# Kernel optimization log

Hardware: AMD Instinct MI355X
Metric: run time of the kernel (lower is better)

Reference implementation:

```python
import jax, jax.numpy as jnp
import numpy as np

EPS = 1e-5  # torch LayerNorm default

def ln(x, g, b):
    mu = jnp.mean(x, axis=-1, keepdims=True)
    var = jnp.mean((x - mu) ** 2, axis=-1, keepdims=True)
    return (x - mu) * jax.lax.rsqrt(var + EPS) * g + b

B, S, E, A = 131072, 199, 3, 32
D_IN = S + 1  # state_dim + 1 (time feature)

def setup_inputs() -> dict:
    key = jax.random.key(0)
    ks = iter(jax.random.split(key, 32))
    def w(shape, fan_in):
        lim = 1.0 / np.sqrt(fan_in)
        return jax.random.uniform(next(ks), shape, jnp.float32, -lim, lim)
    inp = {
        "state": jax.random.normal(next(ks), (B, S), jnp.float32),
        "time_delta": jax.random.uniform(next(ks), (B,), jnp.float32),
        # trunk: Linear(200,256)+LN, Linear(256,256)+LN, Linear(256,128)+LN
        "W1": w((D_IN, 256), D_IN), "b1": w((256,), D_IN),
        "g1": jnp.ones((256,), jnp.float32), "be1": jnp.zeros((256,), jnp.float32),
        "W2": w((256, 256), 256), "b2": w((256,), 256),
        "g2": jnp.ones((256,), jnp.float32), "be2": jnp.zeros((256,), jnp.float32),
        "W3": w((256, 128), 256), "b3": w((128,), 256),
        "g3": jnp.ones((128,), jnp.float32), "be3": jnp.zeros((128,), jnp.float32),
        # value stream
        "Wv1": w((128, 64), 128), "bv1": w((64,), 128),
        "gv": jnp.ones((64,), jnp.float32), "bev": jnp.zeros((64,), jnp.float32),
        "Wv2": w((64, 1), 64), "bv2": w((1,), 64),
        # E stacked advantage streams (all heads share action dim A)
        "Wa1": w((E, 128, 64), 128), "ba1": w((E, 64), 128),
        "ga": jnp.ones((E, 64), jnp.float32), "bea": jnp.zeros((E, 64), jnp.float32),
        "Wa2": w((E, 64, A), 64), "ba2": w((E, A), 64),
        "event_type": jax.random.randint(next(ks), (B,), 0, E),
    }
    return inp

def reference(state, time_delta,
              W1, b1, g1, be1, W2, b2, g2, be2, W3, b3, g3, be3,
              Wv1, bv1, gv, bev, Wv2, bv2,
              Wa1, ba1, ga, bea, Wa2, ba2, event_type):
    td = time_delta[:, None]                       # [B,1]
    x = jnp.concatenate([state, td], axis=1)       # [B,200]
    h = jax.nn.relu(ln(x @ W1 + b1, g1, be1))      # [B,256]
    h = jax.nn.relu(ln(h @ W2 + b2, g2, be2))      # [B,256]
    f = jax.nn.relu(ln(h @ W3 + b3, g3, be3))      # [B,128]
    v = jax.nn.relu(ln(f @ Wv1 + bv1, gv, bev)) @ Wv2 + bv2  # [B,1]
    # compute all E advantage heads, then per-sample select by event_type
    h1 = jnp.einsum('bd,edh->ebh', f, Wa1) + ba1[:, None, :]           # [E,B,64]
    h1 = jax.nn.relu(ln(h1, ga[:, None, :], bea[:, None, :]))
    adv_all = jnp.einsum('ebh,eha->eba', h1, Wa2) + ba2[:, None, :]    # [E,B,A]
    adv = jnp.take_along_axis(adv_all, event_type[None, :, None], axis=0)[0]  # [B,A]
    return v + (adv - adv.mean(axis=1, keepdims=True))
```

## Files before the change

### kernel.cpp

```cpp
#include <hip/hip_runtime.h>
#include <hip/hip_bf16.h>
#include <stdint.h>

#define DEV __device__ __forceinline__

typedef __attribute__((ext_vector_type(8))) short short8;
typedef __attribute__((ext_vector_type(4))) float floatx4;

constexpr int TM  = 64;
constexpr int NB  = 131072;
constexpr int AST = 264;

constexpr int OFF_W1 = 0;
constexpr int OFF_W2 = 57344;
constexpr int OFF_W3 = 122880;
constexpr int OFF_WH = 155648;
constexpr int OFF_WA2= 188416;
constexpr int NWQ    = 194560;

constexpr int C_B1=0, C_G1=256, C_BE1=512, C_B2=768, C_G2=1024, C_BE2=1280,
  C_B3=1536, C_G3=1664, C_BE3=1792, C_BV1=1920, C_GV=1984, C_BEV=2048,
  C_WV2=2112, C_BV2=2176, C_BA1=2180, C_GA=2372, C_BEA=2564, C_BA2=2756;
constexpr int NCONST=2852;

struct Ptrs {
  const float *state,*td,*W1,*b1,*g1,*be1,*W2,*b2,*g2,*be2,*W3,*b3,*g3,*be3,
    *Wv1,*bv1,*gv,*bev,*Wv2,*bv2,*Wa1,*ba1,*ga,*bea,*Wa2,*ba2;
  const int *et;
};

DEV unsigned short f2bf(float x){
  uint32_t u = __float_as_uint(x);
  u += 0x7fffu + ((u>>16)&1u);
  return (unsigned short)(u>>16);
}
DEV uint32_t f2bf_pk(float a, float b){
  float2 f2; f2.x=a; f2.y=b;
  __hip_bfloat162 h = __float22bfloat162_rn(f2);
  union { __hip_bfloat162 h; uint32_t u; } cv; cv.h = h;
  return cv.u;
}

__global__ void prep_kernel(Ptrs p, unsigned short* __restrict__ wq, float* __restrict__ cq){
  int idx = blockIdx.x*256 + threadIdx.x;
  if (idx < NWQ) {
    float v = 0.f;
    if (idx < OFF_W2) {
      int e = idx, w = e/14336, r = e%14336;
      int kc = r>>11, ct=(r>>9)&3, l=(r>>3)&63, j=r&7;
      int n = w*64 + ct*16 + (l&15);
      int k = kc*32 + (l>>4)*8 + j;
      if (k < 200) v = p.W1[k*256 + n];
      else if (k == 200) v = p.b1[n];
    } else if (idx < OFF_W3) {
      int e = idx-OFF_W2, w=e>>14, r=e&16383;
      int kc=r>>11, ct=(r>>9)&3, l=(r>>3)&63, j=r&7;
      int n = w*64 + ct*16 + (l&15);
      int k = kc*32 + (l>>4)*8 + j;
      v = p.W2[k*256 + n];
    } else if (idx < OFF_WH) {
      int e = idx-OFF_W3, w=e>>13, r=e&8191;
      int kc=r>>10, ct=(r>>9)&1, l=(r>>3)&63, j=r&7;
      int n = w*32 + ct*16 + (l&15);
      int k = kc*32 + (l>>4)*8 + j;
      v = p.W3[k*128 + n];
    } else if (idx < OFF_WA2) {
      int e = idx-OFF_WH, h=e>>13, r=e&8191;
      int kc=r>>11, ct=(r>>9)&3, l=(r>>3)&63, j=r&7;
      int n = ct*16 + (l&15);
      int k = kc*32 + (l>>4)*8 + j;
      v = (h<3) ? p.Wa1[h*8192 + k*64 + n] : p.Wv1[k*64 + n];
    } else {
      int e = idx-OFF_WA2, h=e>>11, r=e&2047;
      int kc=r>>10, ct=(r>>9)&1, l=(r>>3)&63, j=r&7;
      int n = ct*16 + (l&15);
      int k = kc*32 + (l>>4)*8 + j;
      v = p.Wa2[h*2048 + k*32 + n];
    }
    wq[idx] = f2bf(v);
  } else if (idx < NWQ + NCONST) {
    int ci = idx - NWQ;
    float v;
    if      (ci < 256)  v = p.b1[ci];
    else if (ci < 512)  v = p.g1[ci-256];
    else if (ci < 768)  v = p.be1[ci-512];
    else if (ci < 1024) v = p.b2[ci-768];
    else if (ci < 1280) v = p.g2[ci-1024];
    else if (ci < 1536) v = p.be2[ci-1280];
    else if (ci < 1664) v = p.b3[ci-1536];
    else if (ci < 1792) v = p.g3[ci-1664];
    else if (ci < 1920) v = p.be3[ci-1792];
    else if (ci < 1984) v = p.bv1[ci-1920];
    else if (ci < 2048) v = p.gv[ci-1984];
    else if (ci < 2112) v = p.bev[ci-2048];
    else if (ci < 2176) v = p.Wv2[ci-2112];
    else if (ci < 2180) v = (ci==2176) ? p.bv2[0] : 0.f;
    else if (ci < 2372) v = p.ba1[ci-2180];
    else if (ci < 2564) v = p.ga[ci-2372];
    else if (ci < 2756) v = p.bea[ci-2564];
    else                v = p.ba2[ci-2756];
    cq[ci] = v;
  }
}

template<int RT,int CT>
DEV void zeroAccT(floatx4 (&acc)[RT][CT]){
  const floatx4 z = {0.f,0.f,0.f,0.f};
  #pragma unroll
  for (int rt=0;rt<RT;rt++)
    #pragma unroll
    for (int ct=0;ct<CT;ct++) acc[rt][ct]=z;
}

template<int KC,int RT,int CT>
DEV void runGemmTW(floatx4 (&acc)[RT][CT], const unsigned short* __restrict__ wp, int kcStride,
                   const unsigned short* aB, int aOff, int lane){
  #pragma unroll
  for (int kc=0;kc<KC;kc++){
    short8 a[CT];
    #pragma unroll
    for (int c=0;c<CT;c++)
      a[c] = *(const short8*)(aB + c*16*AST + aOff + kc*32);
    #pragma unroll
    for (int rt=0;rt<RT;rt++){
      short8 bw = *(const short8*)(wp + kc*kcStride + rt*512 + lane*8);
      #pragma unroll
      for (int c=0;c<CT;c++)
        acc[rt][c] = __builtin_amdgcn_mfma_f32_16x16x32_bf16(bw, a[c], acc[rt][c], 0,0,0);
    }
  }
}

template<int RT,bool BIAS>
DEV void statsT(floatx4 (&acc)[RT][4], const float* __restrict__ cq, int bo,
                float* sbuf, float* ssbuf, int q, int ln){
  if constexpr (BIAS){
    #pragma unroll
    for (int rt=0;rt<RT;rt++){
      floatx4 b4 = *(const floatx4*)(cq + bo + rt*16 + q*4);
      #pragma unroll
      for (int ct=0;ct<4;ct++) acc[rt][ct] += b4;
    }
  }
  #pragma unroll
  for (int ct=0;ct<4;ct++){
    float s=0.f, ss=0.f;
    #pragma unroll
    for (int rt=0;rt<RT;rt++)
      #pragma unroll
      for (int r=0;r<4;r++){ float v=acc[rt][ct][r]; s+=v; ss+=v*v; }
    s += __shfl_xor(s,16); ss += __shfl_xor(ss,16);
    s += __shfl_xor(s,32); ss += __shfl_xor(ss,32);
    if (q==0){
      atomicAdd(&sbuf[ct*16+ln], s);
      atomicAdd(&ssbuf[ct*16+ln], ss);
    }
  }
}

template<int RT>
DEV void lnWriteT(const floatx4 (&acc)[RT][4], const float* __restrict__ cq, int go, int beo,
                  const float* sbuf, const float* ssbuf, float invN,
                  unsigned short* act_, int colBase, int q, int ln){
  float mu[4], rs[4];
  #pragma unroll
  for (int ct=0;ct<4;ct++){
    float sv = sbuf[ct*16+ln], ssv = ssbuf[ct*16+ln];
    mu[ct] = sv*invN;
    rs[ct] = rsqrtf(ssv*invN - mu[ct]*mu[ct] + 1e-5f);
  }
  #pragma unroll
  for (int rt=0;rt<RT;rt++){
    floatx4 g4  = *(const floatx4*)(cq + go  + rt*16 + q*4);
    floatx4 be4 = *(const floatx4*)(cq + beo + rt*16 + q*4);
    #pragma unroll
    for (int ct=0;ct<4;ct++){
      float y[4];
      #pragma unroll
      for (int r=0;r<4;r++)
        y[r] = fmaxf((acc[rt][ct][r]-mu[ct])*rs[ct]*g4[r]+be4[r], 0.f);
      uint2 pk; pk.x = f2bf_pk(y[0],y[1]); pk.y = f2bf_pk(y[2],y[3]);
      *(uint2*)(act_ + (ct*16+ln)*AST + colBase + rt*16 + q*4) = pk;
    }
  }
}

__global__ __launch_bounds__(512,6) void dqn_main(
    const float* __restrict__ state, const float* __restrict__ td,
    const int* __restrict__ et, const unsigned short* __restrict__ wq,
    const float* __restrict__ cq, float* __restrict__ out)
{
  __shared__ __align__(16) unsigned short act[TM*AST];
  __shared__ float sstat[2][2][64];
  __shared__ float vbuf[64];
  __shared__ int   etl[64];

  const int tid=threadIdx.x, w=tid>>6, lane=tid&63, q=lane>>4, ln=lane&15;
  const int rowBlk = blockIdx.x*TM;

  {
    if (tid < 256) ((float*)sstat)[tid] = 0.f;
    const float* sbase = state + (size_t)rowBlk*199;
    #pragma unroll
    for (int it=0; it<4; ++it){
      int t = tid + it*512;
      if (t < 1792){
        int r = t/28, c = t - r*28;
        unsigned short* dst = act + r*AST + c*8;
        if (c < 25){
          const float* src = sbase + r*199 + c*8;
          float v0=src[0], v1=src[1], v2=src[2], v3=src[3];
          float v4=src[4], v5=src[5], v6=src[6];
          int o7 = (c==24)? 198 : c*8+7;
          float s7 = sbase[r*199 + o7];
          float v7 = (c==24)? td[rowBlk+r] : s7;
          uint4 pk;
          pk.x=f2bf_pk(v0,v1); pk.y=f2bf_pk(v2,v3);
          pk.z=f2bf_pk(v4,v5); pk.w=f2bf_pk(v6,v7);
          *(uint4*)dst = pk;
        } else {
          uint4 pk{0u,0u,0u,0u};
          if (c==25) pk.x = 0x3F80u;
          *(uint4*)dst = pk;
        }
      }
    }
    if (tid < 64) etl[tid] = et[rowBlk+tid];
  }
  __syncthreads();

  const unsigned short* aBase = act + ln*AST + q*8;
  floatx4 acc[2][4];

  {
    const unsigned short* wp = wq + OFF_W1 + (w>>1)*14336 + (w&1)*1024;
    zeroAccT<2,4>(acc);
    runGemmTW<7,2,4>(acc, wp, 2048, aBase, 0, lane);
  }
  statsT<2,false>(acc, cq, 0, sstat[0][0], sstat[0][1], q, ln);
  __syncthreads();
  lnWriteT<2>(acc, cq, C_G1+w*32, C_BE1+w*32, sstat[0][0], sstat[0][1], 1.f/256.f, act, w*32, q, ln);
  __syncthreads();

  {
    const unsigned short* wp = wq + OFF_W2 + (w>>1)*16384 + (w&1)*1024;
    zeroAccT<2,4>(acc);
    runGemmTW<8,2,4>(acc, wp, 2048, aBase, 0, lane);
  }
  statsT<2,true>(acc, cq, C_B2+w*32, sstat[1][0], sstat[1][1], q, ln);
  __syncthreads();
  if (tid < 128) ((float*)sstat[0])[tid] = 0.f;
  lnWriteT<2>(acc, cq, C_G2+w*32, C_BE2+w*32, sstat[1][0], sstat[1][1], 1.f/256.f, act, w*32, q, ln);
  __syncthreads();

  floatx4 acc3[1][4];
  {
    const unsigned short* wp = wq + OFF_W3 + (w>>1)*8192 + (w&1)*512;
    zeroAccT<1,4>(acc3);
    runGemmTW<8,1,4>(acc3, wp, 1024, aBase, 0, lane);
  }
  statsT<1,true>(acc3, cq, C_B3+w*16, sstat[0][0], sstat[0][1], q, ln);
  __syncthreads();
  lnWriteT<1>(acc3, cq, C_G3+w*16, C_BE3+w*16, sstat[0][0], sstat[0][1], 1.f/128.f, act, w*16, q, ln);
  __syncthreads();

  const int h = w>>1, bh = w&1;
  const unsigned short* aBaseH = act + (bh*32 + ln)*AST + q*8;
  floatx4 acch[4][2];
  {
    const unsigned short* wp = wq + OFF_WH + h*8192;
    zeroAccT<4,2>(acch);
    runGemmTW<4,4,2>(acch, wp, 2048, aBaseH, 0, lane);
  }
  {
    const int bo = (h<3)? C_BA1+h*64 : C_BV1;
    const int go = (h<3)? C_GA +h*64 : C_GV;
    const int beo= (h<3)? C_BEA+h*64 : C_BEV;
    #pragma unroll
    for (int rt=0;rt<4;rt++){
      floatx4 b4 = *(const floatx4*)(cq + bo + rt*16 + q*4);
      #pragma unroll
      for (int ct=0;ct<2;ct++) acch[rt][ct] += b4;
    }
    float mu[2], rs[2];
    #pragma unroll
    for (int ct=0;ct<2;ct++){
      float s=0.f, ss=0.f;
      #pragma unroll
      for (int rt=0;rt<4;rt++)
        #pragma unroll
        for (int r=0;r<4;r++){ float v=acch[rt][ct][r]; s+=v; ss+=v*v; }
      s += __shfl_xor(s,16); ss += __shfl_xor(ss,16);
      s += __shfl_xor(s,32); ss += __shfl_xor(ss,32);
      mu[ct]=s*(1.f/64.f);
      rs[ct]=rsqrtf(ss*(1.f/64.f)-mu[ct]*mu[ct]+1e-5f);
    }
    #pragma unroll
    for (int rt=0;rt<4;rt++){
      floatx4 g4  = *(const floatx4*)(cq + go  + rt*16 + q*4);
      floatx4 be4 = *(const floatx4*)(cq + beo + rt*16 + q*4);
      #pragma unroll
      for (int ct=0;ct<2;ct++)
        #pragma unroll
        for (int r=0;r<4;r++)
          acch[rt][ct][r] = fmaxf((acch[rt][ct][r]-mu[ct])*rs[ct]*g4[r]+be4[r], 0.f);
    }
    if (h==3){
      float bv2v = cq[C_BV2];
      floatx4 wv4[4];
      #pragma unroll
      for (int rt=0;rt<4;rt++) wv4[rt] = *(const floatx4*)(cq + C_WV2 + rt*16 + q*4);
      #pragma unroll
      for (int ct=0;ct<2;ct++){
        float dot=0.f;
        #pragma unroll
        for (int rt=0;rt<4;rt++)
          #pragma unroll
          for (int r=0;r<4;r++) dot += acch[rt][ct][r]*wv4[rt][r];
        dot += __shfl_xor(dot,16);
        dot += __shfl_xor(dot,32);
        if (q==0) vbuf[(bh*2+ct)*16+ln] = dot + bv2v;
      }
    }
  }
  __syncthreads();

  if (h<3){
    #pragma unroll
    for (int rt=0;rt<4;rt++)
      #pragma unroll
      for (int ct=0;ct<2;ct++){
        uint2 pk;
        pk.x = f2bf_pk(acch[rt][ct][0], acch[rt][ct][1]);
        pk.y = f2bf_pk(acch[rt][ct][2], acch[rt][ct][3]);
        *(uint2*)(act + ((bh*2+ct)*16+ln)*AST + 64*h + rt*16 + q*4) = pk;
      }
    floatx4 acc2[2][2];
    {
      const unsigned short* wp = wq + OFF_WA2 + h*2048;
      zeroAccT<2,2>(acc2);
      runGemmTW<2,2,2>(acc2, wp, 1024, aBaseH, 64*h, lane);
    }
    #pragma unroll
    for (int rt=0;rt<2;rt++){
      floatx4 b4 = *(const floatx4*)(cq + C_BA2 + h*32 + rt*16 + q*4);
      #pragma unroll
      for (int ct=0;ct<2;ct++) acc2[rt][ct] += b4;
    }
    #pragma unroll
    for (int ct=0;ct<2;ct++){
      float sm=0.f;
      #pragma unroll
      for (int rt=0;rt<2;rt++)
        #pragma unroll
        for (int r=0;r<4;r++) sm += acc2[rt][ct][r];
      sm += __shfl_xor(sm,16);
      sm += __shfl_xor(sm,32);
      int b = (bh*2+ct)*16+ln;
      if (etl[b]==h){
        float vm = vbuf[b] - sm*(1.f/32.f);
        #pragma unroll
        for (int rt=0;rt<2;rt++){
          floatx4 o = acc2[rt][ct];
          o[0]+=vm; o[1]+=vm; o[2]+=vm; o[3]+=vm;
          *(floatx4*)(out + (size_t)(rowBlk+b)*32 + rt*16 + q*4) = o;
        }
      }
    }
  }
}

extern "C" void kernel_launch(void* const* d_in, const int* in_sizes, int n_in,
                              void* d_out, int out_size, void* d_ws, size_t ws_size,
                              hipStream_t stream)
{
  Ptrs p;
  p.state=(const float*)d_in[0];  p.td =(const float*)d_in[1];
  p.W1 =(const float*)d_in[2];  p.b1 =(const float*)d_in[3];  p.g1 =(const float*)d_in[4];  p.be1=(const float*)d_in[5];
  p.W2 =(const float*)d_in[6];  p.b2 =(const float*)d_in[7];  p.g2 =(const float*)d_in[8];  p.be2=(const float*)d_in[9];
  p.W3 =(const float*)d_in[10]; p.b3 =(const float*)d_in[11]; p.g3 =(const float*)d_in[12]; p.be3=(const float*)d_in[13];
  p.Wv1=(const float*)d_in[14]; p.bv1=(const float*)d_in[15]; p.gv =(const float*)d_in[16]; p.bev=(const float*)d_in[17];
  p.Wv2=(const float*)d_in[18]; p.bv2=(const float*)d_in[19];
  p.Wa1=(const float*)d_in[20]; p.ba1=(const float*)d_in[21]; p.ga =(const float*)d_in[22]; p.bea=(const float*)d_in[23];
  p.Wa2=(const float*)d_in[24]; p.ba2=(const float*)d_in[25];
  p.et =(const int*)d_in[26];

  unsigned short* wq = (unsigned short*)d_ws;
  float* cq = (float*)((char*)d_ws + (size_t)NWQ*2);

  const int prepN = NWQ + NCONST;
  hipLaunchKernelGGL(prep_kernel, dim3((prepN+255)/256), dim3(256), 0, stream, p, wq, cq);
  hipLaunchKernelGGL(dqn_main, dim3(NB/TM), dim3(512), 0, stream,
                     p.state, p.td, p.et, (const unsigned short*)wq, (const float*)cq, (float*)d_out);
}
```

Before: 287.0 us.

## Rewrite MLP as register-resident per-wave 32-row pipeline using 32x32 MFMA

Replaces the block-cooperative LDS-staged design with one where each wave owns 32 batch rows and keeps activations entirely in registers. Layers use 32x32x16 bf16 MFMA, with LayerNorm stats reduced within the wave, and permlane32 swaps repack outputs into B fragments for the next layer. Biases are folded into the weight matrices as an extra K row. This removes LDS round-trips, atomics and block barriers between layers, at the cost of heavy register pressure at 2 blocks of 256 threads and every wave streaming the full weight set from global/L2.

```diff
diff --git a/kernel.cpp b/kernel.cpp
--- a/kernel.cpp
+++ b/kernel.cpp
@@ -5,23 +5,21 @@
 #define DEV __device__ __forceinline__
 
 typedef __attribute__((ext_vector_type(8))) short short8;
+typedef __attribute__((ext_vector_type(16))) float f32x16;
 typedef __attribute__((ext_vector_type(4))) float floatx4;
 
-constexpr int TM  = 64;
-constexpr int NB  = 131072;
-constexpr int AST = 264;
+constexpr int NB = 131072;
 
 constexpr int OFF_W1 = 0;
-constexpr int OFF_W2 = 57344;
+constexpr int OFF_W2 = 53248;
 constexpr int OFF_W3 = 122880;
-constexpr int OFF_WH = 155648;
-constexpr int OFF_WA2= 188416;
-constexpr int NWQ    = 194560;
-
-constexpr int C_B1=0, C_G1=256, C_BE1=512, C_B2=768, C_G2=1024, C_BE2=1280,
-  C_B3=1536, C_G3=1664, C_BE3=1792, C_BV1=1920, C_GV=1984, C_BEV=2048,
-  C_WV2=2112, C_BV2=2176, C_BA1=2180, C_GA=2372, C_BEA=2564, C_BA2=2756;
-constexpr int NCONST=2852;
+constexpr int OFF_WH = 157696;
+constexpr int OFF_WA2= 194560;
+constexpr int NWQ    = 202240;
+
+constexpr int C_G1=0, C_BE1=256, C_G2=512, C_BE2=768, C_G3=1024, C_BE3=1152,
+  C_GH=1280, C_BEH=1536, C_WV2=1792, C_BV2=1856;
+constexpr int NCONST=1860;
 
 struct Ptrs {
   const float *state,*td,*W1,*b1,*g1,*be1,*W2,*b2,*g2,*be2,*W3,*b3,*g3,*be3,
@@ -34,7 +32,7 @@
   u += 0x7fffu + ((u>>16)&1u);
   return (unsigned short)(u>>16);
 }
-DEV uint32_t f2bf_pk(float a, float b){
+DEV uint32_t pkbf(float a, float b){
   float2 f2; f2.x=a; f2.y=b;
   __hip_bfloat162 h = __float22bfloat162_rn(f2);
   union { __hip_bfloat162 h; uint32_t u; } cv; cv.h = h;
@@ -46,325 +44,318 @@
   if (idx < NWQ) {
     float v = 0.f;
     if (idx < OFF_W2) {
-      int e = idx, w = e/14336, r = e%14336;
-      int kc = r>>11, ct=(r>>9)&3, l=(r>>3)&63, j=r&7;
-      int n = w*64 + ct*16 + (l&15);
-      int k = kc*32 + (l>>4)*8 + j;
+      int e=idx, kc=e>>12, li=e&4095, nt=li>>9, l=(li>>3)&63, j=li&7;
+      int k = kc*16 + (l>>5)*8 + j, n = nt*32 + (l&31);
       if (k < 200) v = p.W1[k*256 + n];
       else if (k == 200) v = p.b1[n];
     } else if (idx < OFF_W3) {
-      int e = idx-OFF_W2, w=e>>14, r=e&16383;
-      int kc=r>>11, ct=(r>>9)&3, l=(r>>3)&63, j=r&7;
-      int n = w*64 + ct*16 + (l&15);
-      int k = kc*32 + (l>>4)*8 + j;
-      v = p.W2[k*256 + n];
+      int e=idx-OFF_W2, kc=e>>12, li=e&4095, nt=li>>9, l=(li>>3)&63, j=li&7;
+      int k = kc*16 + (l>>5)*8 + j, n = nt*32 + (l&31);
+      if (k < 256) v = p.W2[k*256 + n];
+      else if (k == 256) v = p.b2[n];
     } else if (idx < OFF_WH) {
-      int e = idx-OFF_W3, w=e>>13, r=e&8191;
-      int kc=r>>10, ct=(r>>9)&1, l=(r>>3)&63, j=r&7;
-      int n = w*32 + ct*16 + (l&15);
-      int k = kc*32 + (l>>4)*8 + j;
-      v = p.W3[k*128 + n];
+      int e=idx-OFF_W3, kc=e>>11, li=e&2047, nt=li>>9, l=(li>>3)&63, j=li&7;
+      int k = kc*16 + (l>>5)*8 + j, n = nt*32 + (l&31);
+      if (k < 256) v = p.W3[k*128 + n];
+      else if (k == 256) v = p.b3[n];
     } else if (idx < OFF_WA2) {
-      int e = idx-OFF_WH, h=e>>13, r=e&8191;
-      int kc=r>>11, ct=(r>>9)&3, l=(r>>3)&63, j=r&7;
-      int n = ct*16 + (l&15);
-      int k = kc*32 + (l>>4)*8 + j;
-      v = (h<3) ? p.Wa1[h*8192 + k*64 + n] : p.Wv1[k*64 + n];
+      int e=idx-OFF_WH, kc=e>>12, li=e&4095, nt=li>>9, l=(li>>3)&63, j=li&7;
+      int k = kc*16 + (l>>5)*8 + j;
+      int h = nt>>1, nl = (nt&1)*32 + (l&31);
+      if (k < 128) v = (h<3) ? p.Wa1[h*8192 + k*64 + nl] : p.Wv1[k*64 + nl];
+      else if (k == 128) v = (h<3) ? p.ba1[h*64 + nl] : p.bv1[nl];
     } else {
-      int e = idx-OFF_WA2, h=e>>11, r=e&2047;
-      int kc=r>>10, ct=(r>>9)&1, l=(r>>3)&63, j=r&7;
-      int n = ct*16 + (l&15);
-      int k = kc*32 + (l>>4)*8 + j;
-      v = p.Wa2[h*2048 + k*32 + n];
+      int e=idx-OFF_WA2, kc=e/1536, li=e%1536, h=li>>9, l=(li>>3)&63, j=li&7;
+      int k = kc*16 + (l>>5)*8 + j, nl = l&31;
+      if (k < 64) v = p.Wa2[h*2048 + k*32 + nl];
+      else if (k == 64) v = p.ba2[h*32 + nl];
     }
     wq[idx] = f2bf(v);
   } else if (idx < NWQ + NCONST) {
-    int ci = idx - NWQ;
-    float v;
-    if      (ci < 256)  v = p.b1[ci];
-    else if (ci < 512)  v = p.g1[ci-256];
-    else if (ci < 768)  v = p.be1[ci-512];
-    else if (ci < 1024) v = p.b2[ci-768];
-    else if (ci < 1280) v = p.g2[ci-1024];
-    else if (ci < 1536) v = p.be2[ci-1280];
-    else if (ci < 1664) v = p.b3[ci-1536];
-    else if (ci < 1792) v = p.g3[ci-1664];
-    else if (ci < 1920) v = p.be3[ci-1792];
-    else if (ci < 1984) v = p.bv1[ci-1920];
-    else if (ci < 2048) v = p.gv[ci-1984];
-    else if (ci < 2112) v = p.bev[ci-2048];
-    else if (ci < 2176) v = p.Wv2[ci-2112];
-    else if (ci < 2180) v = (ci==2176) ? p.bv2[0] : 0.f;
-    else if (ci < 2372) v = p.ba1[ci-2180];
-    else if (ci < 2564) v = p.ga[ci-2372];
-    else if (ci < 2756) v = p.bea[ci-2564];
-    else                v = p.ba2[ci-2756];
+    int ci = idx - NWQ; float v = 0.f;
+    if      (ci < 256)  v = p.g1[ci];
+    else if (ci < 512)  v = p.be1[ci-256];
+    else if (ci < 768)  v = p.g2[ci-512];
+    else if (ci < 1024) v = p.be2[ci-768];
+    else if (ci < 1152) v = p.g3[ci-1024];
+    else if (ci < 1280) v = p.be3[ci-1152];
+    else if (ci < 1536) { int i=ci-1280; v = (i<192)? p.ga[i]  : p.gv[i-192]; }
+    else if (ci < 1792) { int i=ci-1536; v = (i<192)? p.bea[i] : p.bev[i-192]; }
+    else if (ci < 1856) v = p.Wv2[ci-1792];
+    else if (ci ==1856) v = p.bv2[0];
     cq[ci] = v;
   }
 }
 
-template<int RT,int CT>
-DEV void zeroAccT(floatx4 (&acc)[RT][CT]){
-  const floatx4 z = {0.f,0.f,0.f,0.f};
-  #pragma unroll
-  for (int rt=0;rt<RT;rt++)
-    #pragma unroll
-    for (int ct=0;ct<CT;ct++) acc[rt][ct]=z;
-}
-
-template<int KC,int RT,int CT>
-DEV void runGemmTW(floatx4 (&acc)[RT][CT], const unsigned short* __restrict__ wp, int kcStride,
-                   const unsigned short* aB, int aOff, int lane){
-  #pragma unroll
-  for (int kc=0;kc<KC;kc++){
-    short8 a[CT];
-    #pragma unroll
-    for (int c=0;c<CT;c++)
-      a[c] = *(const short8*)(aB + c*16*AST + aOff + kc*32);
-    #pragma unroll
-    for (int rt=0;rt<RT;rt++){
-      short8 bw = *(const short8*)(wp + kc*kcStride + rt*512 + lane*8);
-      #pragma unroll
-      for (int c=0;c<CT;c++)
-        acc[rt][c] = __builtin_amdgcn_mfma_f32_16x16x32_bf16(bw, a[c], acc[rt][c], 0,0,0);
-    }
-  }
-}
-
-template<int RT,bool BIAS>
-DEV void statsT(floatx4 (&acc)[RT][4], const float* __restrict__ cq, int bo,
-                float* sbuf, float* ssbuf, int q, int ln){
-  if constexpr (BIAS){
-    #pragma unroll
-    for (int rt=0;rt<RT;rt++){
-      floatx4 b4 = *(const floatx4*)(cq + bo + rt*16 + q*4);
-      #pragma unroll
-      for (int ct=0;ct<4;ct++) acc[rt][ct] += b4;
-    }
-  }
-  #pragma unroll
-  for (int ct=0;ct<4;ct++){
-    float s=0.f, ss=0.f;
-    #pragma unroll
-    for (int rt=0;rt<RT;rt++)
-      #pragma unroll
-      for (int r=0;r<4;r++){ float v=acc[rt][ct][r]; s+=v; ss+=v*v; }
-    s += __shfl_xor(s,16); ss += __shfl_xor(ss,16);
-    s += __shfl_xor(s,32); ss += __shfl_xor(ss,32);
-    if (q==0){
-      atomicAdd(&sbuf[ct*16+ln], s);
-      atomicAdd(&ssbuf[ct*16+ln], ss);
-    }
-  }
-}
-
-template<int RT>
-DEV void lnWriteT(const floatx4 (&acc)[RT][4], const float* __restrict__ cq, int go, int beo,
-                  const float* sbuf, const float* ssbuf, float invN,
-                  unsigned short* act_, int colBase, int q, int ln){
-  float mu[4], rs[4];
-  #pragma unroll
-  for (int ct=0;ct<4;ct++){
-    float sv = sbuf[ct*16+ln], ssv = ssbuf[ct*16+ln];
-    mu[ct] = sv*invN;
-    rs[ct] = rsqrtf(ssv*invN - mu[ct]*mu[ct] + 1e-5f);
-  }
-  #pragma unroll
-  for (int rt=0;rt<RT;rt++){
-    floatx4 g4  = *(const floatx4*)(cq + go  + rt*16 + q*4);
-    floatx4 be4 = *(const floatx4*)(cq + beo + rt*16 + q*4);
-    #pragma unroll
-    for (int ct=0;ct<4;ct++){
-      float y[4];
-      #pragma unroll
-      for (int r=0;r<4;r++)
-        y[r] = fmaxf((acc[rt][ct][r]-mu[ct])*rs[ct]*g4[r]+be4[r], 0.f);
-      uint2 pk; pk.x = f2bf_pk(y[0],y[1]); pk.y = f2bf_pk(y[2],y[3]);
-      *(uint2*)(act_ + (ct*16+ln)*AST + colBase + rt*16 + q*4) = pk;
-    }
-  }
-}
-
-__global__ __launch_bounds__(512,6) void dqn_main(
+DEV floatx4 ld4(const float* p){ return *(const floatx4*)p; }
+
+DEV short8 mk_frag(uint32_t w0, uint32_t w1, uint32_t w2, uint32_t w3){
+  union { uint32_t u[4]; short8 s; } cv;
+  cv.u[0]=w0; cv.u[1]=w1; cv.u[2]=w2; cv.u[3]=w3; return cv.s;
+}
+DEV void pl32swap(uint32_t &x, uint32_t &y){
+  asm volatile("v_permlane32_swap_b32 %0, %1" : "+v"(x), "+v"(y));
+}
+DEV f32x16 mf(short8 a, short8 b, f32x16 c){
+  return __builtin_amdgcn_mfma_f32_32x32x16_bf16(a, b, c, 0, 0, 0);
+}
+
+DEV void tile_to_frags(const float (&y)[16], short8 &f0, short8 &f1){
+  uint32_t P0 = pkbf(y[0], y[1]), P1 = pkbf(y[2], y[3]);
+  uint32_t Q0 = pkbf(y[4], y[5]), Q1 = pkbf(y[6], y[7]);
+  pl32swap(P0, Q0); pl32swap(P1, Q1);
+  f0 = mk_frag(P0, P1, Q0, Q1);
+  uint32_t R0 = pkbf(y[8], y[9]),  R1 = pkbf(y[10], y[11]);
+  uint32_t S0 = pkbf(y[12], y[13]),S1 = pkbf(y[14], y[15]);
+  pl32swap(R0, S0); pl32swap(R1, S1);
+  f1 = mk_frag(R0, R1, S0, S1);
+}
+
+__global__ __launch_bounds__(256,2) void dqn_main(
     const float* __restrict__ state, const float* __restrict__ td,
     const int* __restrict__ et, const unsigned short* __restrict__ wq,
     const float* __restrict__ cq, float* __restrict__ out)
 {
-  __shared__ __align__(16) unsigned short act[TM*AST];
-  __shared__ float sstat[2][2][64];
-  __shared__ float vbuf[64];
-  __shared__ int   etl[64];
-
-  const int tid=threadIdx.x, w=tid>>6, lane=tid&63, q=lane>>4, ln=lane&15;
-  const int rowBlk = blockIdx.x*TM;
-
-  {
-    if (tid < 256) ((float*)sstat)[tid] = 0.f;
-    const float* sbase = state + (size_t)rowBlk*199;
-    #pragma unroll
-    for (int it=0; it<4; ++it){
-      int t = tid + it*512;
-      if (t < 1792){
-        int r = t/28, c = t - r*28;
-        unsigned short* dst = act + r*AST + c*8;
-        if (c < 25){
-          const float* src = sbase + r*199 + c*8;
-          float v0=src[0], v1=src[1], v2=src[2], v3=src[3];
-          float v4=src[4], v5=src[5], v6=src[6];
-          int o7 = (c==24)? 198 : c*8+7;
-          float s7 = sbase[r*199 + o7];
-          float v7 = (c==24)? td[rowBlk+r] : s7;
-          uint4 pk;
-          pk.x=f2bf_pk(v0,v1); pk.y=f2bf_pk(v2,v3);
-          pk.z=f2bf_pk(v4,v5); pk.w=f2bf_pk(v6,v7);
-          *(uint4*)dst = pk;
+  const int tid = threadIdx.x, wv = tid>>6, l = tid&63;
+  const int hi = l>>5, c = l&31;
+  const int b = blockIdx.x*128 + wv*32 + c;
+
+  const float* sph = state + (size_t)b*199 + hi*8;
+  const float  tdv = td[b];
+  const int    etv = et[b];
+
+  const f32x16 z16 = {0,0,0,0,0,0,0,0,0,0,0,0,0,0,0,0};
+  const short8 bias_bf = mk_frag(hi==0 ? 0x3F80u : 0u, 0u, 0u, 0u);
+
+  f32x16 acc[8];
+
+  {
+    #pragma unroll
+    for (int t=0;t<8;t++) acc[t] = z16;
+    const unsigned short* wl = wq + OFF_W1 + l*8;
+    #pragma unroll
+    for (int kc=0;kc<13;kc++){
+      short8 bf;
+      if (kc < 12){
+        float v0=sph[kc*16+0], v1=sph[kc*16+1], v2=sph[kc*16+2], v3=sph[kc*16+3];
+        float v4=sph[kc*16+4], v5=sph[kc*16+5], v6=sph[kc*16+6], v7=sph[kc*16+7];
+        bf = mk_frag(pkbf(v0,v1), pkbf(v2,v3), pkbf(v4,v5), pkbf(v6,v7));
+      } else {
+        if (hi == 0){
+          float v0=sph[192], v1=sph[193], v2=sph[194], v3=sph[195];
+          float v4=sph[196], v5=sph[197], v6=sph[198], v7=tdv;
+          bf = mk_frag(pkbf(v0,v1), pkbf(v2,v3), pkbf(v4,v5), pkbf(v6,v7));
         } else {
-          uint4 pk{0u,0u,0u,0u};
-          if (c==25) pk.x = 0x3F80u;
-          *(uint4*)dst = pk;
-        }
-      }
-    }
-    if (tid < 64) etl[tid] = et[rowBlk+tid];
-  }
-  __syncthreads();
-
-  const unsigned short* aBase = act + ln*AST + q*8;
-  floatx4 acc[2][4];
-
-  {
-    const unsigned short* wp = wq + OFF_W1 + (w>>1)*14336 + (w&1)*1024;
-    zeroAccT<2,4>(acc);
-    runGemmTW<7,2,4>(acc, wp, 2048, aBase, 0, lane);
-  }
-  statsT<2,false>(acc, cq, 0, sstat[0][0], sstat[0][1], q, ln);
-  __syncthreads();
-  lnWriteT<2>(acc, cq, C_G1+w*32, C_BE1+w*32, sstat[0][0], sstat[0][1], 1.f/256.f, act, w*32, q, ln);
-  __syncthreads();
-
-  {
-    const unsigned short* wp = wq + OFF_W2 + (w>>1)*16384 + (w&1)*1024;
-    zeroAccT<2,4>(acc);
-    runGemmTW<8,2,4>(acc, wp, 2048, aBase, 0, lane);
-  }
-  statsT<2,true>(acc, cq, C_B2+w*32, sstat[1][0], sstat[1][1], q, ln);
-  __syncthreads();
-  if (tid < 128) ((float*)sstat[0])[tid] = 0.f;
-  lnWriteT<2>(acc, cq, C_G2+w*32, C_BE2+w*32, sstat[1][0], sstat[1][1], 1.f/256.f, act, w*32, q, ln);
-  __syncthreads();
-
-  floatx4 acc3[1][4];
-  {
-    const unsigned short* wp = wq + OFF_W3 + (w>>1)*8192 + (w&1)*512;
-    zeroAccT<1,4>(acc3);
-    runGemmTW<8,1,4>(acc3, wp, 1024, aBase, 0, lane);
-  }
-  statsT<1,true>(acc3, cq, C_B3+w*16, sstat[0][0], sstat[0][1], q, ln);
-  __syncthreads();
-  lnWriteT<1>(acc3, cq, C_G3+w*16, C_BE3+w*16, sstat[0][0], sstat[0][1], 1.f/128.f, act, w*16, q, ln);
-  __syncthreads();
-
-  const int h = w>>1, bh = w&1;
-  const unsigned short* aBaseH = act + (bh*32 + ln)*AST + q*8;
-  floatx4 acch[4][2];
-  {
-    const unsigned short* wp = wq + OFF_WH + h*8192;
-    zeroAccT<4,2>(acch);
-    runGemmTW<4,4,2>(acch, wp, 2048, aBaseH, 0, lane);
-  }
-  {
-    const int bo = (h<3)? C_BA1+h*64 : C_BV1;
-    const int go = (h<3)? C_GA +h*64 : C_GV;
-    const int beo= (h<3)? C_BEA+h*64 : C_BEV;
-    #pragma unroll
-    for (int rt=0;rt<4;rt++){
-      floatx4 b4 = *(const floatx4*)(cq + bo + rt*16 + q*4);
-      #pragma unroll
-      for (int ct=0;ct<2;ct++) acch[rt][ct] += b4;
-    }
-    float mu[2], rs[2];
-    #pragma unroll
-    for (int ct=0;ct<2;ct++){
-      float s=0.f, ss=0.f;
-      #pragma unroll
-      for (int rt=0;rt<4;rt++)
-        #pragma unroll
-        for (int r=0;r<4;r++){ float v=acch[rt][ct][r]; s+=v; ss+=v*v; }
-      s += __shfl_xor(s,16); ss += __shfl_xor(ss,16);
-      s += __shfl_xor(s,32); ss += __shfl_xor(ss,32);
-      mu[ct]=s*(1.f/64.f);
-      rs[ct]=rsqrtf(ss*(1.f/64.f)-mu[ct]*mu[ct]+1e-5f);
-    }
-    #pragma unroll
-    for (int rt=0;rt<4;rt++){
-      floatx4 g4  = *(const floatx4*)(cq + go  + rt*16 + q*4);
-      floatx4 be4 = *(const floatx4*)(cq + beo + rt*16 + q*4);
-      #pragma unroll
-      for (int ct=0;ct<2;ct++)
-        #pragma unroll
-        for (int r=0;r<4;r++)
-          acch[rt][ct][r] = fmaxf((acch[rt][ct][r]-mu[ct])*rs[ct]*g4[r]+be4[r], 0.f);
-    }
-    if (h==3){
-      float bv2v = cq[C_BV2];
-      floatx4 wv4[4];
-      #pragma unroll
-      for (int rt=0;rt<4;rt++) wv4[rt] = *(const floatx4*)(cq + C_WV2 + rt*16 + q*4);
-      #pragma unroll
-      for (int ct=0;ct<2;ct++){
-        float dot=0.f;
-        #pragma unroll
-        for (int rt=0;rt<4;rt++)
-          #pragma unroll
-          for (int r=0;r<4;r++) dot += acch[rt][ct][r]*wv4[rt][r];
-        dot += __shfl_xor(dot,16);
-        dot += __shfl_xor(dot,32);
-        if (q==0) vbuf[(bh*2+ct)*16+ln] = dot + bv2v;
-      }
-    }
-  }
-  __syncthreads();
-
-  if (h<3){
-    #pragma unroll
-    for (int rt=0;rt<4;rt++)
-      #pragma unroll
-      for (int ct=0;ct<2;ct++){
-        uint2 pk;
-        pk.x = f2bf_pk(acch[rt][ct][0], acch[rt][ct][1]);
-        pk.y = f2bf_pk(acch[rt][ct][2], acch[rt][ct][3]);
-        *(uint2*)(act + ((bh*2+ct)*16+ln)*AST + 64*h + rt*16 + q*4) = pk;
-      }
-    floatx4 acc2[2][2];
-    {
-      const unsigned short* wp = wq + OFF_WA2 + h*2048;
-      zeroAccT<2,2>(acc2);
-      runGemmTW<2,2,2>(acc2, wp, 1024, aBaseH, 64*h, lane);
-    }
-    #pragma unroll
-    for (int rt=0;rt<2;rt++){
-      floatx4 b4 = *(const floatx4*)(cq + C_BA2 + h*32 + rt*16 + q*4);
-      #pragma unroll
-      for (int ct=0;ct<2;ct++) acc2[rt][ct] += b4;
-    }
-    #pragma unroll
-    for (int ct=0;ct<2;ct++){
-      float sm=0.f;
-      #pragma unroll
-      for (int rt=0;rt<2;rt++)
-        #pragma unroll
-        for (int r=0;r<4;r++) sm += acc2[rt][ct][r];
-      sm += __shfl_xor(sm,16);
-      sm += __shfl_xor(sm,32);
-      int b = (bh*2+ct)*16+ln;
-      if (etl[b]==h){
-        float vm = vbuf[b] - sm*(1.f/32.f);
-        #pragma unroll
-        for (int rt=0;rt<2;rt++){
-          floatx4 o = acc2[rt][ct];
-          o[0]+=vm; o[1]+=vm; o[2]+=vm; o[3]+=vm;
-          *(floatx4*)(out + (size_t)(rowBlk+b)*32 + rt*16 + q*4) = o;
-        }
+          bf = mk_frag(0x3F80u, 0u, 0u, 0u);
+        }
+      }
+      #pragma unroll
+      for (int nt=0;nt<8;nt++)
+        acc[nt] = mf(*(const short8*)(wl + (kc*8+nt)*512), bf, acc[nt]);
+    }
+  }
+
+  short8 Bf[16];
+  {
+    float s=0.f, ss=0.f;
+    #pragma unroll
+    for (int t=0;t<8;t++)
+      #pragma unroll
+      for (int r=0;r<16;r++){ float v=acc[t][r]; s+=v; ss+=v*v; }
+    s += __shfl_xor(s,32); ss += __shfl_xor(ss,32);
+    float mu = s*(1.f/256.f);
+    float rsv = rsqrtf(ss*(1.f/256.f) - mu*mu + 1e-5f);
+    float mrs = mu*rsv;
+    #pragma unroll
+    for (int t=0;t<8;t++){
+      float y[16];
+      #pragma unroll
+      for (int m=0;m<4;m++){
+        floatx4 g4 = ld4(cq + C_G1  + t*32 + m*8 + hi*4);
+        floatx4 e4 = ld4(cq + C_BE1 + t*32 + m*8 + hi*4);
+        #pragma unroll
+        for (int rr=0;rr<4;rr++){
+          float tv = fmaf(acc[t][m*4+rr], rsv, -mrs);
+          y[m*4+rr] = fmaxf(fmaf(tv, g4[rr], e4[rr]), 0.f);
+        }
+      }
+      tile_to_frags(y, Bf[t*2], Bf[t*2+1]);
+    }
+  }
+
+  {
+    #pragma unroll
+    for (int t=0;t<8;t++) acc[t] = z16;
+    const unsigned short* wl = wq + OFF_W2 + l*8;
+    #pragma unroll
+    for (int kc=0;kc<17;kc++){
+      short8 bf = (kc<16) ? Bf[kc] : bias_bf;
+      #pragma unroll
+      for (int nt=0;nt<8;nt++)
+        acc[nt] = mf(*(const short8*)(wl + (kc*8+nt)*512), bf, acc[nt]);
+    }
+  }
+
+  {
+    float s=0.f, ss=0.f;
+    #pragma unroll
+    for (int t=0;t<8;t++)
+      #pragma unroll
+      for (int r=0;r<16;r++){ float v=acc[t][r]; s+=v; ss+=v*v; }
+    s += __shfl_xor(s,32); ss += __shfl_xor(ss,32);
+    float mu = s*(1.f/256.f);
+    float rsv = rsqrtf(ss*(1.f/256.f) - mu*mu + 1e-5f);
+    float mrs = mu*rsv;
+    #pragma unroll
+    for (int t=0;t<8;t++){
+      float y[16];
+      #pragma unroll
+      for (int m=0;m<4;m++){
+        floatx4 g4 = ld4(cq + C_G2  + t*32 + m*8 + hi*4);
+        floatx4 e4 = ld4(cq + C_BE2 + t*32 + m*8 + hi*4);
+        #pragma unroll
+        for (int rr=0;rr<4;rr++){
+          float tv = fmaf(acc[t][m*4+rr], rsv, -mrs);
+          y[m*4+rr] = fmaxf(fmaf(tv, g4[rr], e4[rr]), 0.f);
+        }
+      }
+      tile_to_frags(y, Bf[t*2], Bf[t*2+1]);
+    }
+  }
+
+  {
+    #pragma unroll
+    for (int t=0;t<4;t++) acc[t] = z16;
+    const unsigned short* wl = wq + OFF_W3 + l*8;
+    #pragma unroll
+    for (int kc=0;kc<17;kc++){
+      short8 bf = (kc<16) ? Bf[kc] : bias_bf;
+      #pragma unroll
+      for (int nt=0;nt<4;nt++)
+        acc[nt] = mf(*(const short8*)(wl + (kc*4+nt)*512), bf, acc[nt]);
+    }
+  }
+
+  short8 Ff[8];
+  {
+    float s=0.f, ss=0.f;
+    #pragma unroll
+    for (int t=0;t<4;t++)
+      #pragma unroll
+      for (int r=0;r<16;r++){ float v=acc[t][r]; s+=v; ss+=v*v; }
+    s += __shfl_xor(s,32); ss += __shfl_xor(ss,32);
+    float mu = s*(1.f/128.f);
+    float rsv = rsqrtf(ss*(1.f/128.f) - mu*mu + 1e-5f);
+    float mrs = mu*rsv;
+    #pragma unroll
+    for (int t=0;t<4;t++){
+      float y[16];
+      #pragma unroll
+      for (int m=0;m<4;m++){
+        floatx4 g4 = ld4(cq + C_G3  + t*32 + m*8 + hi*4);
+        floatx4 e4 = ld4(cq + C_BE3 + t*32 + m*8 + hi*4);
+        #pragma unroll
+        for (int rr=0;rr<4;rr++){
+          float tv = fmaf(acc[t][m*4+rr], rsv, -mrs);
+          y[m*4+rr] = fmaxf(fmaf(tv, g4[rr], e4[rr]), 0.f);
+        }
+      }
+      tile_to_frags(y, Ff[t*2], Ff[t*2+1]);
+    }
+  }
+
+  {
+    #pragma unroll
+    for (int t=0;t<8;t++) acc[t] = z16;
+    const unsigned short* wl = wq + OFF_WH + l*8;
+    #pragma unroll
+    for (int kc=0;kc<9;kc++){
+      short8 bf = (kc<8) ? Ff[kc] : bias_bf;
+      #pragma unroll
+      for (int nt=0;nt<8;nt++)
+        acc[nt] = mf(*(const short8*)(wl + (kc*8+nt)*512), bf, acc[nt]);
+    }
+  }
+
+  float vval;
+  {
+    float s=0.f, ss=0.f;
+    #pragma unroll
+    for (int t=6;t<8;t++)
+      #pragma unroll
+      for (int r=0;r<16;r++){ float v=acc[t][r]; s+=v; ss+=v*v; }
+    s += __shfl_xor(s,32); ss += __shfl_xor(ss,32);
+    float mu = s*(1.f/64.f);
+    float rsv = rsqrtf(ss*(1.f/64.f) - mu*mu + 1e-5f);
+    float mrs = mu*rsv;
+    float dot = 0.f;
+    #pragma unroll
+    for (int t=6;t<8;t++)
+      #pragma unroll
+      for (int m=0;m<4;m++){
+        floatx4 g4 = ld4(cq + C_GH  + t*32 + m*8 + hi*4);
+        floatx4 e4 = ld4(cq + C_BEH + t*32 + m*8 + hi*4);
+        floatx4 w4 = ld4(cq + C_WV2 + (t-6)*32 + m*8 + hi*4);
+        #pragma unroll
+        for (int rr=0;rr<4;rr++){
+          float tv = fmaf(acc[t][m*4+rr], rsv, -mrs);
+          float y  = fmaxf(fmaf(tv, g4[rr], e4[rr]), 0.f);
+          dot = fmaf(y, w4[rr], dot);
+        }
+      }
+    dot += __shfl_xor(dot,32);
+    vval = dot + cq[C_BV2];
+  }
+
+  const unsigned short* wla = wq + OFF_WA2 + l*8;
+  #pragma unroll
+  for (int h=0;h<3;h++){
+    float s=0.f, ss=0.f;
+    #pragma unroll
+    for (int t2=0;t2<2;t2++){
+      int t = 2*h + t2;
+      #pragma unroll
+      for (int r=0;r<16;r++){ float v=acc[t][r]; s+=v; ss+=v*v; }
+    }
+    s += __shfl_xor(s,32); ss += __shfl_xor(ss,32);
+    float mu = s*(1.f/64.f);
+    float rsv = rsqrtf(ss*(1.f/64.f) - mu*mu + 1e-5f);
+    float mrs = mu*rsv;
+    short8 Hf[4];
+    #pragma unroll
+    for (int t2=0;t2<2;t2++){
+      int t = 2*h + t2;
+      float y[16];
+      #pragma unroll
+      for (int m=0;m<4;m++){
+        floatx4 g4 = ld4(cq + C_GH  + t*32 + m*8 + hi*4);
+        floatx4 e4 = ld4(cq + C_BEH + t*32 + m*8 + hi*4);
+        #pragma unroll
+        for (int rr=0;rr<4;rr++){
+          float tv = fmaf(acc[t][m*4+rr], rsv, -mrs);
+          y[m*4+rr] = fmaxf(fmaf(tv, g4[rr], e4[rr]), 0.f);
+        }
+      }
+      tile_to_frags(y, Hf[t2*2], Hf[t2*2+1]);
+    }
+    f32x16 a2 = z16;
+    #pragma unroll
+    for (int kc=0;kc<5;kc++){
+      short8 bf = (kc<4) ? Hf[kc] : bias_bf;
+      a2 = mf(*(const short8*)(wla + (kc*3+h)*512), bf, a2);
+    }
+    float sm = 0.f;
+    #pragma unroll
+    for (int r=0;r<16;r++) sm += a2[r];
+    sm += __shfl_xor(sm,32);
+    if (etv == h){
+      float vm = vval - sm*(1.f/32.f);
+      #pragma unroll
+      for (int m=0;m<4;m++){
+        floatx4 o;
+        #pragma unroll
+        for (int rr=0;rr<4;rr++) o[rr] = a2[m*4+rr] + vm;
+        *(floatx4*)(out + (size_t)b*32 + m*8 + hi*4) = o;
       }
     }
   }
@@ -390,6 +381,6 @@
 
   const int prepN = NWQ + NCONST;
   hipLaunchKernelGGL(prep_kernel, dim3((prepN+255)/256), dim3(256), 0, stream, p, wq, cq);
-  hipLaunchKernelGGL(dqn_main, dim3(NB/TM), dim3(512), 0, stream,
+  hipLaunchKernelGGL(dqn_main, dim3(NB/128), dim3(256), 0, stream,
                      p.state, p.td, p.et, (const unsigned short*)wq, (const float*)cq, (float*)d_out);
 }
```

New measurement: 329.1 us. 1.15x slower.
